# Performance work log

Measured on AMD Instinct MI355X. Metric: run time of the kernel, lower is better.

The kernel has to match this reference:

```python
import jax, jax.numpy as jnp
import numpy as np

B, L, D, H = 2, 2048, 1024, 16
HD = D // H


def setup_inputs() -> dict:
    key = jax.random.key(0)
    ks = jax.random.split(key, 5)
    # xavier-uniform-ish scale for DxD linears
    scale = float(np.sqrt(6.0 / (D + D)))
    def lin_w(k):
        return jax.random.uniform(k, (D, D), jnp.float32, -scale, scale)
    return {
        "x": jax.random.normal(ks[0], (B, L, D), jnp.float32),
        "wq": lin_w(ks[1]), "bq": jnp.zeros((D,), jnp.float32),
        "wk": lin_w(ks[2]), "bk": jnp.zeros((D,), jnp.float32),
        "wv": lin_w(ks[3]), "bv": jnp.zeros((D,), jnp.float32),
        "wo": lin_w(ks[4]), "bo": jnp.zeros((D,), jnp.float32),
    }


def reference(x, wq, bq, wk, bk, wv, bv, wo, bo):
    b, l, d = x.shape
    # projections: torch Linear is x @ W.T + b
    def split_heads(t):
        return t.reshape(b, l, H, HD).transpose(0, 2, 1, 3)  # (B,H,L,HD)
    Q = split_heads(x @ wq.T + bq)
    K = split_heads(x @ wk.T + bk)
    V = split_heads(x @ wv.T + bv)
    scores = jnp.einsum("bhqd,bhkd->bhqk", Q, K) / jnp.sqrt(jnp.asarray(HD, x.dtype))
    attn = jax.nn.softmax(scores, axis=-1)  # (B,H,L,L)
    out = jnp.einsum("bhqk,bhkd->bhqd", attn, V)
    out = out.transpose(0, 2, 1, 3).reshape(b, l, d)
    return out @ wo.T + bo
```

## Files before the change

kernel.cpp:

```cpp
#include <hip/hip_runtime.h>
#include <hip/hip_bf16.h>
#include <cstdint>

#define LEN   2048
#define DMODEL 1024
#define NH    16
#define HD    64
#define BH    32
#define MROWS 4096

typedef __attribute__((ext_vector_type(8))) short bf16x8;
typedef __attribute__((ext_vector_type(4))) float f32x4;
typedef unsigned int u32;

__device__ __forceinline__ void gload_lds16(const void* g, void* l) {
    __builtin_amdgcn_global_load_lds(
        (const __attribute__((address_space(1))) u32*)g,
        (__attribute__((address_space(3))) u32*)l, 16, 0, 0);
}

__device__ __forceinline__ unsigned short bfb(float f) {
    __hip_bfloat16 h = __float2bfloat16(f);
    return *reinterpret_cast<unsigned short*>(&h);
}

__global__ void cast_f32_bf16_k(const float* __restrict__ in,
                                __hip_bfloat16* __restrict__ out, int n4) {
    int stride = gridDim.x * blockDim.x;
    for (int i = blockIdx.x * blockDim.x + threadIdx.x; i < n4; i += stride) {
        float4 v = reinterpret_cast<const float4*>(in)[i];
        ushort4 p;
        p.x = bfb(v.x); p.y = bfb(v.y); p.z = bfb(v.z); p.w = bfb(v.w);
        reinterpret_cast<ushort4*>(out)[i] = p;
    }
}

__global__ __launch_bounds__(256) void gemm_qkv(
    const __hip_bfloat16* __restrict__ A,
    const __hip_bfloat16* __restrict__ Bw,
    const float* __restrict__ bq, const float* __restrict__ bk,
    const float* __restrict__ bv,
    __hip_bfloat16* __restrict__ Qb, __hip_bfloat16* __restrict__ Kb,
    __hip_bfloat16* __restrict__ VTb) {
    constexpr int Kd = DMODEL;
    __shared__ __hip_bfloat16 As[128 * 32];
    __shared__ __hip_bfloat16 Bs[128 * 32];
    const int tid = threadIdx.x;
    const int wave = tid >> 6, lane = tid & 63;
    const int lg = lane >> 4, lr = lane & 15;
    const int wr = wave >> 1, wc = wave & 1;
    const int by = blockIdx.y, bx = blockIdx.x;
    const __hip_bfloat16* Ab = A + (size_t)by * 128 * Kd;
    const __hip_bfloat16* Bb = Bw + (size_t)bx * 128 * Kd;
    f32x4 acc[4][4] = {};
    for (int kt = 0; kt < Kd / 32; ++kt) {
#pragma unroll
        for (int i = 0; i < 2; ++i) {
            int c = tid + i * 256;
            int row = c >> 2, c4 = c & 3;
            gload_lds16(Ab + (size_t)row * Kd + kt * 32 + c4 * 8, &As[c * 8]);
        }
#pragma unroll
        for (int i = 0; i < 2; ++i) {
            int c = tid + i * 256;
            int row = c >> 2, c4 = c & 3;
            gload_lds16(Bb + (size_t)row * Kd + kt * 32 + c4 * 8, &Bs[c * 8]);
        }
        __syncthreads();
        bf16x8 af[4], bfr[4];
#pragma unroll
        for (int m = 0; m < 4; ++m)
            af[m] = *(const bf16x8*)&As[(wr * 64 + m * 16 + lr) * 32 + lg * 8];
#pragma unroll
        for (int n = 0; n < 4; ++n)
            bfr[n] = *(const bf16x8*)&Bs[(wc * 64 + n * 16 + lr) * 32 + lg * 8];
#pragma unroll
        for (int m = 0; m < 4; ++m)
#pragma unroll
            for (int n = 0; n < 4; ++n)
                acc[m][n] = __builtin_amdgcn_mfma_f32_16x16x32_bf16(
                    af[m], bfr[n], acc[m][n], 0, 0, 0);
        __syncthreads();
    }
    const int sel = (bx * 128) >> 10;
    const float* bp = sel == 0 ? bq : (sel == 1 ? bk : bv);
    __hip_bfloat16* dst = sel == 0 ? Qb : (sel == 1 ? Kb : VTb);
#pragma unroll
    for (int m = 0; m < 4; ++m)
#pragma unroll
        for (int n = 0; n < 4; ++n)
#pragma unroll
            for (int r = 0; r < 4; ++r) {
                int gm = by * 128 + wr * 64 + m * 16 + lg * 4 + r;
                int gn = bx * 128 + wc * 64 + n * 16 + lr;
                int nn = gn & (DMODEL - 1);
                float v = acc[m][n][r] + bp[nn];
                int bb = gm >> 11, l = gm & (LEN - 1);
                int h = nn >> 6, hd = nn & (HD - 1);
                size_t addr = (sel < 2)
                    ? ((((size_t)bb * NH + h) * LEN + l) * HD + hd)
                    : ((((size_t)bb * NH + h) * HD + hd) * LEN + l);
                dst[addr] = __float2bfloat16(v);
            }
}

#define SC 0.18033688f
__global__ __launch_bounds__(256) void attn_fwd(
    const __hip_bfloat16* __restrict__ Qb,
    const __hip_bfloat16* __restrict__ Kb,
    const __hip_bfloat16* __restrict__ VTb,
    __hip_bfloat16* __restrict__ Ob) {
    const int lin = blockIdx.x;
    const int wg = (lin & 7) * 128 + (lin >> 3);
    const int bh = wg >> 5;
    const int qt = wg & 31;
    const int b = bh >> 4, h = bh & (NH - 1);
    const int tid = threadIdx.x;
    const int wave = tid >> 6, lane = tid & 63;
    const int lg = lane >> 4, lr = lane & 15;
    const int sw = lr & 7;
    const int qw = qt * 64 + wave * 16;
    const __hip_bfloat16* Qp = Qb + ((size_t)bh * LEN + qw) * HD;
    const __hip_bfloat16* Kp = Kb + (size_t)bh * LEN * HD;
    const __hip_bfloat16* Vp = VTb + (size_t)bh * HD * LEN;

    __shared__ __hip_bfloat16 Ks[2][64 * 64];
    __shared__ __hip_bfloat16 Vs[2][64 * 64];
    __shared__ __hip_bfloat16 Plds[4][16][72];
    __hip_bfloat16* pl = &Plds[wave][0][0];

    const int c0 = tid, c1 = tid + 256;
    const int r0 = c0 >> 3, j0 = (c0 & 7) ^ (r0 & 7);
    const int r1 = c1 >> 3, j1 = (c1 & 7) ^ (r1 & 7);
    const __hip_bfloat16* kg0 = Kp + (size_t)r0 * HD + j0 * 8;
    const __hip_bfloat16* kg1 = Kp + (size_t)r1 * HD + j1 * 8;
    const __hip_bfloat16* vg0 = Vp + (size_t)r0 * LEN + j0 * 8;
    const __hip_bfloat16* vg1 = Vp + (size_t)r1 * LEN + j1 * 8;

    bf16x8 qf[2];
    qf[0] = *(const bf16x8*)(Qp + lr * HD + lg * 8);
    qf[1] = *(const bf16x8*)(Qp + lr * HD + 32 + lg * 8);

    float m_i = -INFINITY;
    float l_i = 0.f;
    f32x4 o[4] = {};

    gload_lds16(kg0, &Ks[0][c0 * 8]);
    gload_lds16(kg1, &Ks[0][c1 * 8]);
    gload_lds16(vg0, &Vs[0][c0 * 8]);
    gload_lds16(vg1, &Vs[0][c1 * 8]);
    __syncthreads();

    constexpr int NT = LEN / 64;
    for (int kt = 0; kt < NT; ++kt) {
        const int cb = kt & 1, nb = cb ^ 1;
        if (kt + 1 < NT) {
            size_t ko = (size_t)(kt + 1) * 64 * HD;
            size_t vo = (size_t)(kt + 1) * 64;
            gload_lds16(kg0 + ko, &Ks[nb][c0 * 8]);
            gload_lds16(kg1 + ko, &Ks[nb][c1 * 8]);
            gload_lds16(vg0 + vo, &Vs[nb][c0 * 8]);
            gload_lds16(vg1 + vo, &Vs[nb][c1 * 8]);
        }
        const __hip_bfloat16* ks = Ks[cb];
        const __hip_bfloat16* vs = Vs[cb];
        f32x4 s[4] = {};
#pragma unroll
        for (int kk = 0; kk < 2; ++kk) {
#pragma unroll
            for (int n = 0; n < 4; ++n) {
                int krow = n * 16 + lr;
                bf16x8 kf = *(const bf16x8*)&ks[krow * 64 +
                                                (((kk << 2) + lg) ^ sw) * 8];
                s[n] = __builtin_amdgcn_mfma_f32_16x16x32_bf16(kf, qf[kk], s[n],
                                                               0, 0, 0);
            }
        }
        float t0 = fmaxf(fmaxf(s[0][0], s[0][1]), fmaxf(s[0][2], s[0][3]));
        float t1 = fmaxf(fmaxf(s[1][0], s[1][1]), fmaxf(s[1][2], s[1][3]));
        float t2 = fmaxf(fmaxf(s[2][0], s[2][1]), fmaxf(s[2][2], s[2][3]));
        float t3 = fmaxf(fmaxf(s[3][0], s[3][1]), fmaxf(s[3][2], s[3][3]));
        float tmax = fmaxf(fmaxf(t0, t1), fmaxf(t2, t3));
        tmax = fmaxf(tmax, __shfl_xor(tmax, 16, 64));
        tmax = fmaxf(tmax, __shfl_xor(tmax, 32, 64));
        float pmax = tmax * SC;
        if (__any(pmax > m_i + 8.f)) {
            float mnew = fmaxf(m_i, pmax);
            float corr = exp2f(m_i - mnew);
            m_i = mnew;
            l_i *= corr;
#pragma unroll
            for (int r = 0; r < 4; ++r) {
                float cr = __shfl(corr, lg * 4 + r, 16);
#pragma unroll
                for (int n = 0; n < 4; ++n) o[n][r] *= cr;
            }
        }
        float p[4][4];
#pragma unroll
        for (int n = 0; n < 4; ++n)
#pragma unroll
            for (int r = 0; r < 4; ++r)
                p[n][r] = exp2f(s[n][r] * SC - m_i);
        float a0 = (p[0][0] + p[0][1]) + (p[0][2] + p[0][3]);
        float a1 = (p[1][0] + p[1][1]) + (p[1][2] + p[1][3]);
        float a2 = (p[2][0] + p[2][1]) + (p[2][2] + p[2][3]);
        float a3 = (p[3][0] + p[3][1]) + (p[3][2] + p[3][3]);
        float ps = (a0 + a1) + (a2 + a3);
        ps += __shfl_xor(ps, 16, 64);
        ps += __shfl_xor(ps, 32, 64);
        l_i += ps;
#pragma unroll
        for (int n = 0; n < 4; ++n) {
            ushort4 pk;
            pk.x = bfb(p[n][0]); pk.y = bfb(p[n][1]);
            pk.z = bfb(p[n][2]); pk.w = bfb(p[n][3]);
            *(ushort4*)&pl[lr * 72 + n * 16 + lg * 4] = pk;
        }
        asm volatile("" ::: "memory");
#pragma unroll
        for (int kk = 0; kk < 2; ++kk) {
            bf16x8 pa = *(const bf16x8*)&pl[lr * 72 + kk * 32 + lg * 8];
#pragma unroll
            for (int n = 0; n < 4; ++n) {
                int vrow = n * 16 + lr;
                bf16x8 vf = *(const bf16x8*)&vs[vrow * 64 +
                                                (((kk << 2) + lg) ^ sw) * 8];
                o[n] = __builtin_amdgcn_mfma_f32_16x16x32_bf16(pa, vf, o[n],
                                                               0, 0, 0);
            }
        }
        __syncthreads();
    }
#pragma unroll
    for (int r = 0; r < 4; ++r) {
        float lq = __shfl(l_i, lg * 4 + r, 16);
        float invq = 1.f / lq;
        int gq = qw + lg * 4 + r;
#pragma unroll
        for (int n = 0; n < 4; ++n) {
            int gd = h * HD + n * 16 + lr;
            Ob[((size_t)b * LEN + gq) * DMODEL + gd] =
                __float2bfloat16(o[n][r] * invq);
        }
    }
}

__global__ __launch_bounds__(256) void gemm_out(
    const __hip_bfloat16* __restrict__ A,
    const __hip_bfloat16* __restrict__ Bw,
    const float* __restrict__ bo, float* __restrict__ out) {
    constexpr int Kd = DMODEL, N = DMODEL;
    __shared__ __hip_bfloat16 As[64 * 32];
    __shared__ __hip_bfloat16 Bs[128 * 32];
    const int tid = threadIdx.x;
    const int wave = tid >> 6, lane = tid & 63;
    const int lg = lane >> 4, lr = lane & 15;
    const int wr = wave >> 1, wc = wave & 1;
    const int by = blockIdx.y, bx = blockIdx.x;
    const __hip_bfloat16* Ab = A + (size_t)by * 64 * Kd;
    const __hip_bfloat16* Bb = Bw + (size_t)bx * 128 * Kd;
    f32x4 acc[2][4] = {};
    for (int kt = 0; kt < Kd / 32; ++kt) {
        {
            int c = tid;
            int row = c >> 2, c4 = c & 3;
            gload_lds16(Ab + (size_t)row * Kd + kt * 32 + c4 * 8, &As[c * 8]);
        }
#pragma unroll
        for (int i = 0; i < 2; ++i) {
            int c = tid + i * 256;
            int row = c >> 2, c4 = c & 3;
            gload_lds16(Bb + (size_t)row * Kd + kt * 32 + c4 * 8, &Bs[c * 8]);
        }
        __syncthreads();
        bf16x8 af[2], bfr[4];
#pragma unroll
        for (int m = 0; m < 2; ++m)
            af[m] = *(const bf16x8*)&As[(wr * 32 + m * 16 + lr) * 32 + lg * 8];
#pragma unroll
        for (int n = 0; n < 4; ++n)
            bfr[n] = *(const bf16x8*)&Bs[(wc * 64 + n * 16 + lr) * 32 + lg * 8];
#pragma unroll
        for (int m = 0; m < 2; ++m)
#pragma unroll
            for (int n = 0; n < 4; ++n)
                acc[m][n] = __builtin_amdgcn_mfma_f32_16x16x32_bf16(
                    af[m], bfr[n], acc[m][n], 0, 0, 0);
        __syncthreads();
    }
#pragma unroll
    for (int m = 0; m < 2; ++m)
#pragma unroll
        for (int n = 0; n < 4; ++n)
#pragma unroll
            for (int r = 0; r < 4; ++r) {
                int gm = by * 64 + wr * 32 + m * 16 + lg * 4 + r;
                int gn = bx * 128 + wc * 64 + n * 16 + lr;
                out[(size_t)gm * N + gn] = acc[m][n][r] + bo[gn];
            }
}

extern "C" void kernel_launch(void* const* d_in, const int* in_sizes, int n_in,
                              void* d_out, int out_size, void* d_ws, size_t ws_size,
                              hipStream_t stream) {
    const float* x  = (const float*)d_in[0];
    const float* wq = (const float*)d_in[1];
    const float* bq = (const float*)d_in[2];
    const float* wk = (const float*)d_in[3];
    const float* bk = (const float*)d_in[4];
    const float* wv = (const float*)d_in[5];
    const float* bv = (const float*)d_in[6];
    const float* wo = (const float*)d_in[7];
    const float* bo = (const float*)d_in[8];

    char* ws = (char*)d_ws;
    __hip_bfloat16* x_bf  = (__hip_bfloat16*)(ws);
    __hip_bfloat16* wqkv  = (__hip_bfloat16*)(ws + (8u  << 20));
    __hip_bfloat16* wo_bf = (__hip_bfloat16*)(ws + (14u << 20));
    __hip_bfloat16* Qb    = (__hip_bfloat16*)(ws + (16u << 20));
    __hip_bfloat16* Kb    = (__hip_bfloat16*)(ws + (24u << 20));
    __hip_bfloat16* VTb   = (__hip_bfloat16*)(ws + (32u << 20));
    __hip_bfloat16* Ob    = (__hip_bfloat16*)(ws + (40u << 20));

    cast_f32_bf16_k<<<1024, 256, 0, stream>>>(x, x_bf, (MROWS * DMODEL) / 4);
    cast_f32_bf16_k<<<512, 256, 0, stream>>>(wq, wqkv, (DMODEL * DMODEL) / 4);
    cast_f32_bf16_k<<<512, 256, 0, stream>>>(wk, wqkv + (1u << 20), (DMODEL * DMODEL) / 4);
    cast_f32_bf16_k<<<512, 256, 0, stream>>>(wv, wqkv + (2u << 20), (DMODEL * DMODEL) / 4);
    cast_f32_bf16_k<<<512, 256, 0, stream>>>(wo, wo_bf, (DMODEL * DMODEL) / 4);

    gemm_qkv<<<dim3(24, 32), 256, 0, stream>>>(x_bf, wqkv, bq, bk, bv, Qb, Kb, VTb);
    attn_fwd<<<1024, 256, 0, stream>>>(Qb, Kb, VTb, Ob);
    gemm_out<<<dim3(8, 64), 256, 0, stream>>>(Ob, wo_bf, bo, (float*)d_out);
}
```

Measured before the change: 245.2 us.

## Use 32x32 MFMA in attention, fuse casts, remap GEMM grids with priority hints

Attention now uses 32x32x16 bf16 MFMA with 128-query tiles per block, so each wave handles 32 query rows and K/V tiles loaded into LDS are reused across more queries. The five cast launches are merged into one kernel, and the output GEMM moves to 128x128 tiles. Both GEMMs get an XCD-aware block-index remap, and s_setprio is raised around the MFMA sections. The trade is more registers per wave and fewer blocks in the grid, which may lower occupancy.

```diff
diff --git a/kernel.cpp b/kernel.cpp
--- a/kernel.cpp
+++ b/kernel.cpp
@@ -11,6 +11,7 @@
 
 typedef __attribute__((ext_vector_type(8))) short bf16x8;
 typedef __attribute__((ext_vector_type(4))) float f32x4;
+typedef __attribute__((ext_vector_type(16))) float f32x16;
 typedef unsigned int u32;
 
 __device__ __forceinline__ void gload_lds16(const void* g, void* l) {
@@ -24,14 +25,34 @@
     return *reinterpret_cast<unsigned short*>(&h);
 }
 
-__global__ void cast_f32_bf16_k(const float* __restrict__ in,
-                                __hip_bfloat16* __restrict__ out, int n4) {
+__device__ __forceinline__ u32 pk2(float lo, float hi) {
+    return (u32)bfb(lo) | ((u32)bfb(hi) << 16);
+}
+
+__global__ void cast_all_k(const float* __restrict__ x,
+                           const float* __restrict__ wq, const float* __restrict__ wk,
+                           const float* __restrict__ wv, const float* __restrict__ wo,
+                           __hip_bfloat16* __restrict__ x_bf,
+                           __hip_bfloat16* __restrict__ wqkv,
+                           __hip_bfloat16* __restrict__ wo_bf) {
+    constexpr int XC = 1048576;
+    constexpr int WC = 262144;
+    constexpr int TC = XC + 4 * WC;
     int stride = gridDim.x * blockDim.x;
-    for (int i = blockIdx.x * blockDim.x + threadIdx.x; i < n4; i += stride) {
-        float4 v = reinterpret_cast<const float4*>(in)[i];
+    for (int i = blockIdx.x * blockDim.x + threadIdx.x; i < TC; i += stride) {
+        const float* src; __hip_bfloat16* dst; int so, do_;
+        if (i < XC) { src = x; dst = x_bf; so = i; do_ = i; }
+        else {
+            int j = i - XC, w = j >> 18, o = j & (WC - 1);
+            src = w == 0 ? wq : (w == 1 ? wk : (w == 2 ? wv : wo));
+            so = o;
+            if (w < 3) { dst = wqkv; do_ = j; }
+            else       { dst = wo_bf; do_ = o; }
+        }
+        float4 v = reinterpret_cast<const float4*>(src)[so];
         ushort4 p;
         p.x = bfb(v.x); p.y = bfb(v.y); p.z = bfb(v.z); p.w = bfb(v.w);
-        reinterpret_cast<ushort4*>(out)[i] = p;
+        reinterpret_cast<ushort4*>(dst)[do_] = p;
     }
 }
 
@@ -45,11 +66,13 @@
     constexpr int Kd = DMODEL;
     __shared__ __hip_bfloat16 As[128 * 32];
     __shared__ __hip_bfloat16 Bs[128 * 32];
+    const int lin = blockIdx.x;
+    const int wg = (lin & 7) * 96 + (lin >> 3);
+    const int by = wg / 24, bx = wg % 24;
     const int tid = threadIdx.x;
     const int wave = tid >> 6, lane = tid & 63;
     const int lg = lane >> 4, lr = lane & 15;
     const int wr = wave >> 1, wc = wave & 1;
-    const int by = blockIdx.y, bx = blockIdx.x;
     const __hip_bfloat16* Ab = A + (size_t)by * 128 * Kd;
     const __hip_bfloat16* Bb = Bw + (size_t)bx * 128 * Kd;
     f32x4 acc[4][4] = {};
@@ -74,12 +97,14 @@
 #pragma unroll
         for (int n = 0; n < 4; ++n)
             bfr[n] = *(const bf16x8*)&Bs[(wc * 64 + n * 16 + lr) * 32 + lg * 8];
+        __builtin_amdgcn_s_setprio(1);
 #pragma unroll
         for (int m = 0; m < 4; ++m)
 #pragma unroll
             for (int n = 0; n < 4; ++n)
                 acc[m][n] = __builtin_amdgcn_mfma_f32_16x16x32_bf16(
                     af[m], bfr[n], acc[m][n], 0, 0, 0);
+        __builtin_amdgcn_s_setprio(0);
         __syncthreads();
     }
     const int sel = (bx * 128) >> 10;
@@ -111,23 +136,22 @@
     const __hip_bfloat16* __restrict__ VTb,
     __hip_bfloat16* __restrict__ Ob) {
     const int lin = blockIdx.x;
-    const int wg = (lin & 7) * 128 + (lin >> 3);
-    const int bh = wg >> 5;
-    const int qt = wg & 31;
+    const int wg = (lin & 7) * 64 + (lin >> 3);
+    const int bh = wg >> 4;
+    const int qt = wg & 15;
     const int b = bh >> 4, h = bh & (NH - 1);
     const int tid = threadIdx.x;
     const int wave = tid >> 6, lane = tid & 63;
-    const int lg = lane >> 4, lr = lane & 15;
-    const int sw = lr & 7;
-    const int qw = qt * 64 + wave * 16;
+    const int l31 = lane & 31, hi = lane >> 5;
+    const int qw = qt * 128 + wave * 32;
     const __hip_bfloat16* Qp = Qb + ((size_t)bh * LEN + qw) * HD;
     const __hip_bfloat16* Kp = Kb + (size_t)bh * LEN * HD;
     const __hip_bfloat16* Vp = VTb + (size_t)bh * HD * LEN;
 
     __shared__ __hip_bfloat16 Ks[2][64 * 64];
     __shared__ __hip_bfloat16 Vs[2][64 * 64];
-    __shared__ __hip_bfloat16 Plds[4][16][72];
-    __hip_bfloat16* pl = &Plds[wave][0][0];
+    __shared__ __hip_bfloat16 Pl[4][32][72];
+    __hip_bfloat16* prow = &Pl[wave][l31][0];
 
     const int c0 = tid, c1 = tid + 256;
     const int r0 = c0 >> 3, j0 = (c0 & 7) ^ (r0 & 7);
@@ -137,13 +161,14 @@
     const __hip_bfloat16* vg0 = Vp + (size_t)r0 * LEN + j0 * 8;
     const __hip_bfloat16* vg1 = Vp + (size_t)r1 * LEN + j1 * 8;
 
-    bf16x8 qf[2];
-    qf[0] = *(const bf16x8*)(Qp + lr * HD + lg * 8);
-    qf[1] = *(const bf16x8*)(Qp + lr * HD + 32 + lg * 8);
+    bf16x8 qf[4];
+#pragma unroll
+    for (int ks = 0; ks < 4; ++ks)
+        qf[ks] = *(const bf16x8*)(Qp + l31 * HD + ks * 16 + hi * 8);
 
     float m_i = -INFINITY;
     float l_i = 0.f;
-    f32x4 o[4] = {};
+    f32x16 o[2] = {};
 
     gload_lds16(kg0, &Ks[0][c0 * 8]);
     gload_lds16(kg1, &Ks[0][c1 * 8]);
@@ -151,6 +176,7 @@
     gload_lds16(vg1, &Vs[0][c1 * 8]);
     __syncthreads();
 
+    const int swz = l31 & 7;
     constexpr int NT = LEN / 64;
     for (int kt = 0; kt < NT; ++kt) {
         const int cb = kt & 1, nb = cb ^ 1;
@@ -162,27 +188,28 @@
             gload_lds16(vg0 + vo, &Vs[nb][c0 * 8]);
             gload_lds16(vg1 + vo, &Vs[nb][c1 * 8]);
         }
-        const __hip_bfloat16* ks = Ks[cb];
-        const __hip_bfloat16* vs = Vs[cb];
-        f32x4 s[4] = {};
-#pragma unroll
-        for (int kk = 0; kk < 2; ++kk) {
-#pragma unroll
-            for (int n = 0; n < 4; ++n) {
-                int krow = n * 16 + lr;
-                bf16x8 kf = *(const bf16x8*)&ks[krow * 64 +
-                                                (((kk << 2) + lg) ^ sw) * 8];
-                s[n] = __builtin_amdgcn_mfma_f32_16x16x32_bf16(kf, qf[kk], s[n],
-                                                               0, 0, 0);
-            }
-        }
-        float t0 = fmaxf(fmaxf(s[0][0], s[0][1]), fmaxf(s[0][2], s[0][3]));
-        float t1 = fmaxf(fmaxf(s[1][0], s[1][1]), fmaxf(s[1][2], s[1][3]));
-        float t2 = fmaxf(fmaxf(s[2][0], s[2][1]), fmaxf(s[2][2], s[2][3]));
-        float t3 = fmaxf(fmaxf(s[3][0], s[3][1]), fmaxf(s[3][2], s[3][3]));
-        float tmax = fmaxf(fmaxf(t0, t1), fmaxf(t2, t3));
-        tmax = fmaxf(tmax, __shfl_xor(tmax, 16, 64));
-        tmax = fmaxf(tmax, __shfl_xor(tmax, 32, 64));
+        const __hip_bfloat16* ksp = Ks[cb];
+        const __hip_bfloat16* vsp = Vs[cb];
+        f32x16 s0 = {}, s1 = {};
+        __builtin_amdgcn_s_setprio(1);
+#pragma unroll
+        for (int ks = 0; ks < 4; ++ks) {
+            int ch = ((ks << 1) + hi);
+            bf16x8 kf0 = *(const bf16x8*)&ksp[l31 * 64 + (ch ^ swz) * 8];
+            bf16x8 kf1 = *(const bf16x8*)&ksp[(32 + l31) * 64 + (ch ^ swz) * 8];
+            s0 = __builtin_amdgcn_mfma_f32_32x32x16_bf16(kf0, qf[ks], s0, 0, 0, 0);
+            s1 = __builtin_amdgcn_mfma_f32_32x32x16_bf16(kf1, qf[ks], s1, 0, 0, 0);
+        }
+        __builtin_amdgcn_s_setprio(0);
+        float mx[16];
+#pragma unroll
+        for (int r = 0; r < 16; ++r) mx[r] = fmaxf(s0[r], s1[r]);
+#pragma unroll
+        for (int st = 8; st > 0; st >>= 1)
+#pragma unroll
+            for (int r = 0; r < 8; ++r)
+                if (r < st) mx[r] = fmaxf(mx[r], mx[r + st]);
+        float tmax = fmaxf(mx[0], __shfl_xor(mx[0], 32, 64));
         float pmax = tmax * SC;
         if (__any(pmax > m_i + 8.f)) {
             float mnew = fmaxf(m_i, pmax);
@@ -190,59 +217,61 @@
             m_i = mnew;
             l_i *= corr;
 #pragma unroll
-            for (int r = 0; r < 4; ++r) {
-                float cr = __shfl(corr, lg * 4 + r, 16);
-#pragma unroll
-                for (int n = 0; n < 4; ++n) o[n][r] *= cr;
+            for (int r = 0; r < 16; ++r) {
+                float cr = __shfl(corr, (r & 3) + 8 * (r >> 2) + 4 * hi, 32);
+                o[0][r] *= cr;
+                o[1][r] *= cr;
             }
         }
-        float p[4][4];
-#pragma unroll
-        for (int n = 0; n < 4; ++n)
-#pragma unroll
-            for (int r = 0; r < 4; ++r)
-                p[n][r] = exp2f(s[n][r] * SC - m_i);
-        float a0 = (p[0][0] + p[0][1]) + (p[0][2] + p[0][3]);
-        float a1 = (p[1][0] + p[1][1]) + (p[1][2] + p[1][3]);
-        float a2 = (p[2][0] + p[2][1]) + (p[2][2] + p[2][3]);
-        float a3 = (p[3][0] + p[3][1]) + (p[3][2] + p[3][3]);
-        float ps = (a0 + a1) + (a2 + a3);
-        ps += __shfl_xor(ps, 16, 64);
-        ps += __shfl_xor(ps, 32, 64);
-        l_i += ps;
-#pragma unroll
-        for (int n = 0; n < 4; ++n) {
-            ushort4 pk;
-            pk.x = bfb(p[n][0]); pk.y = bfb(p[n][1]);
-            pk.z = bfb(p[n][2]); pk.w = bfb(p[n][3]);
-            *(ushort4*)&pl[lr * 72 + n * 16 + lg * 4] = pk;
+#pragma unroll
+        for (int r = 0; r < 16; ++r) {
+            s0[r] = exp2f(s0[r] * SC - m_i);
+            s1[r] = exp2f(s1[r] * SC - m_i);
+        }
+        float sm[16];
+#pragma unroll
+        for (int r = 0; r < 16; ++r) sm[r] = s0[r] + s1[r];
+#pragma unroll
+        for (int st = 8; st > 0; st >>= 1)
+#pragma unroll
+            for (int r = 0; r < 8; ++r)
+                if (r < st) sm[r] += sm[r + st];
+        l_i += sm[0] + __shfl_xor(sm[0], 32, 64);
+#pragma unroll
+        for (int g = 0; g < 4; ++g) {
+            uint2 w0, w1;
+            w0.x = pk2(s0[4 * g + 0], s0[4 * g + 1]);
+            w0.y = pk2(s0[4 * g + 2], s0[4 * g + 3]);
+            w1.x = pk2(s1[4 * g + 0], s1[4 * g + 1]);
+            w1.y = pk2(s1[4 * g + 2], s1[4 * g + 3]);
+            *(uint2*)&prow[8 * g + 4 * hi]      = w0;
+            *(uint2*)&prow[32 + 8 * g + 4 * hi] = w1;
         }
         asm volatile("" ::: "memory");
-#pragma unroll
-        for (int kk = 0; kk < 2; ++kk) {
-            bf16x8 pa = *(const bf16x8*)&pl[lr * 72 + kk * 32 + lg * 8];
-#pragma unroll
-            for (int n = 0; n < 4; ++n) {
-                int vrow = n * 16 + lr;
-                bf16x8 vf = *(const bf16x8*)&vs[vrow * 64 +
-                                                (((kk << 2) + lg) ^ sw) * 8];
-                o[n] = __builtin_amdgcn_mfma_f32_16x16x32_bf16(pa, vf, o[n],
-                                                               0, 0, 0);
-            }
-        }
-        __syncthreads();
-    }
-#pragma unroll
-    for (int r = 0; r < 4; ++r) {
-        float lq = __shfl(l_i, lg * 4 + r, 16);
-        float invq = 1.f / lq;
-        int gq = qw + lg * 4 + r;
-#pragma unroll
-        for (int n = 0; n < 4; ++n) {
-            int gd = h * HD + n * 16 + lr;
-            Ob[((size_t)b * LEN + gq) * DMODEL + gd] =
-                __float2bfloat16(o[n][r] * invq);
-        }
+        bf16x8 pa[4];
+#pragma unroll
+        for (int ks = 0; ks < 4; ++ks)
+            pa[ks] = *(const bf16x8*)&prow[ks * 16 + hi * 8];
+        __builtin_amdgcn_s_setprio(1);
+#pragma unroll
+        for (int ks = 0; ks < 4; ++ks) {
+            int ch = ((ks << 1) + hi);
+            bf16x8 vf0 = *(const bf16x8*)&vsp[l31 * 64 + (ch ^ swz) * 8];
+            bf16x8 vf1 = *(const bf16x8*)&vsp[(32 + l31) * 64 + (ch ^ swz) * 8];
+            o[0] = __builtin_amdgcn_mfma_f32_32x32x16_bf16(pa[ks], vf0, o[0], 0, 0, 0);
+            o[1] = __builtin_amdgcn_mfma_f32_32x32x16_bf16(pa[ks], vf1, o[1], 0, 0, 0);
+        }
+        __builtin_amdgcn_s_setprio(0);
+        __syncthreads();
+    }
+#pragma unroll
+    for (int r = 0; r < 16; ++r) {
+        int q = (r & 3) + 8 * (r >> 2) + 4 * hi;
+        float inv = 1.f / __shfl(l_i, q, 32);
+        int gq = qw + q;
+        size_t base = ((size_t)b * LEN + gq) * DMODEL + h * HD + l31;
+        Ob[base]      = __float2bfloat16(o[0][r] * inv);
+        Ob[base + 32] = __float2bfloat16(o[1][r] * inv);
     }
 }
 
@@ -251,19 +280,22 @@
     const __hip_bfloat16* __restrict__ Bw,
     const float* __restrict__ bo, float* __restrict__ out) {
     constexpr int Kd = DMODEL, N = DMODEL;
-    __shared__ __hip_bfloat16 As[64 * 32];
+    __shared__ __hip_bfloat16 As[128 * 32];
     __shared__ __hip_bfloat16 Bs[128 * 32];
+    const int lin = blockIdx.x;
+    const int wg = (lin & 7) * 32 + (lin >> 3);
+    const int by = wg >> 3, bx = wg & 7;
     const int tid = threadIdx.x;
     const int wave = tid >> 6, lane = tid & 63;
     const int lg = lane >> 4, lr = lane & 15;
     const int wr = wave >> 1, wc = wave & 1;
-    const int by = blockIdx.y, bx = blockIdx.x;
-    const __hip_bfloat16* Ab = A + (size_t)by * 64 * Kd;
+    const __hip_bfloat16* Ab = A + (size_t)by * 128 * Kd;
     const __hip_bfloat16* Bb = Bw + (size_t)bx * 128 * Kd;
-    f32x4 acc[2][4] = {};
+    f32x4 acc[4][4] = {};
     for (int kt = 0; kt < Kd / 32; ++kt) {
-        {
-            int c = tid;
+#pragma unroll
+        for (int i = 0; i < 2; ++i) {
+            int c = tid + i * 256;
             int row = c >> 2, c4 = c & 3;
             gload_lds16(Ab + (size_t)row * Kd + kt * 32 + c4 * 8, &As[c * 8]);
         }
@@ -274,28 +306,30 @@
             gload_lds16(Bb + (size_t)row * Kd + kt * 32 + c4 * 8, &Bs[c * 8]);
         }
         __syncthreads();
-        bf16x8 af[2], bfr[4];
-#pragma unroll
-        for (int m = 0; m < 2; ++m)
-            af[m] = *(const bf16x8*)&As[(wr * 32 + m * 16 + lr) * 32 + lg * 8];
+        bf16x8 af[4], bfr[4];
+#pragma unroll
+        for (int m = 0; m < 4; ++m)
+            af[m] = *(const bf16x8*)&As[(wr * 64 + m * 16 + lr) * 32 + lg * 8];
 #pragma unroll
         for (int n = 0; n < 4; ++n)
             bfr[n] = *(const bf16x8*)&Bs[(wc * 64 + n * 16 + lr) * 32 + lg * 8];
-#pragma unroll
-        for (int m = 0; m < 2; ++m)
+        __builtin_amdgcn_s_setprio(1);
+#pragma unroll
+        for (int m = 0; m < 4; ++m)
 #pragma unroll
             for (int n = 0; n < 4; ++n)
                 acc[m][n] = __builtin_amdgcn_mfma_f32_16x16x32_bf16(
                     af[m], bfr[n], acc[m][n], 0, 0, 0);
-        __syncthreads();
-    }
-#pragma unroll
-    for (int m = 0; m < 2; ++m)
+        __builtin_amdgcn_s_setprio(0);
+        __syncthreads();
+    }
+#pragma unroll
+    for (int m = 0; m < 4; ++m)
 #pragma unroll
         for (int n = 0; n < 4; ++n)
 #pragma unroll
             for (int r = 0; r < 4; ++r) {
-                int gm = by * 64 + wr * 32 + m * 16 + lg * 4 + r;
+                int gm = by * 128 + wr * 64 + m * 16 + lg * 4 + r;
                 int gn = bx * 128 + wc * 64 + n * 16 + lr;
                 out[(size_t)gm * N + gn] = acc[m][n][r] + bo[gn];
             }
@@ -323,13 +357,8 @@
     __hip_bfloat16* VTb   = (__hip_bfloat16*)(ws + (32u << 20));
     __hip_bfloat16* Ob    = (__hip_bfloat16*)(ws + (40u << 20));
 
-    cast_f32_bf16_k<<<1024, 256, 0, stream>>>(x, x_bf, (MROWS * DMODEL) / 4);
-    cast_f32_bf16_k<<<512, 256, 0, stream>>>(wq, wqkv, (DMODEL * DMODEL) / 4);
-    cast_f32_bf16_k<<<512, 256, 0, stream>>>(wk, wqkv + (1u << 20), (DMODEL * DMODEL) / 4);
-    cast_f32_bf16_k<<<512, 256, 0, stream>>>(wv, wqkv + (2u << 20), (DMODEL * DMODEL) / 4);
-    cast_f32_bf16_k<<<512, 256, 0, stream>>>(wo, wo_bf, (DMODEL * DMODEL) / 4);
-
-    gemm_qkv<<<dim3(24, 32), 256, 0, stream>>>(x_bf, wqkv, bq, bk, bv, Qb, Kb, VTb);
-    attn_fwd<<<1024, 256, 0, stream>>>(Qb, Kb, VTb, Ob);
-    gemm_out<<<dim3(8, 64), 256, 0, stream>>>(Ob, wo_bf, bo, (float*)d_out);
-}
+    cast_all_k<<<1024, 256, 0, stream>>>(x, wq, wk, wv, wo, x_bf, wqkv, wo_bf);
+    gemm_qkv<<<768, 256, 0, stream>>>(x_bf, wqkv, bq, bk, bv, Qb, Kb, VTb);
+    attn_fwd<<<512, 256, 0, stream>>>(Qb, Kb, VTb, Ob);
+    gemm_out<<<256, 256, 0, stream>>>(Ob, wo_bf, bo, (float*)d_out);
+}
```

Result: faster. 228.8 us (-6.7%).
